# Kernel optimization log

Hardware: AMD Instinct MI355X
Metric: run time of the kernel (lower is better)

Reference implementation:

```python
import jax, jax.numpy as jnp
import numpy as np
from jax import lax

B, N, D, H, E, K, FF = 4, 1024, 1024, 16, 12, 2, 4
HD = D // H
EPS_LN = 1e-5


def setup_inputs() -> dict:
    key = jax.random.key(0)
    ks = jax.random.split(key, 10)
    s = 0.02
    return {
        "x": jax.random.normal(ks[0], (B, N, D), jnp.float32),
        "Wr": jax.random.normal(ks[1], (E, D), jnp.float32) * s,          # router [E, D] (no bias)
        "Wq": jax.random.normal(ks[2], (E, D, D), jnp.float32) * s,       # per-expert [out, in]
        "Wk": jax.random.normal(ks[3], (E, D, D), jnp.float32) * s,
        "Wv": jax.random.normal(ks[4], (E, D, D), jnp.float32) * s,
        "Wo": jax.random.normal(ks[5], (E, D, D), jnp.float32) * s,
        "W1": jax.random.normal(ks[6], (FF * D, D), jnp.float32) * s,
        "b1": jnp.zeros((FF * D,), jnp.float32),
        "W2": jax.random.normal(ks[7], (D, FF * D), jnp.float32) * s,
        "b2": jnp.zeros((D,), jnp.float32),
        "g1": jnp.ones((D,), jnp.float32),
        "be1": jnp.zeros((D,), jnp.float32),
        "g2": jnp.ones((D,), jnp.float32),
        "be2": jnp.zeros((D,), jnp.float32),
    }


def _ln(x, g, b):
    m = jnp.mean(x, axis=-1, keepdims=True)
    v = jnp.mean(jnp.square(x - m), axis=-1, keepdims=True)
    return (x - m) * lax.rsqrt(v + EPS_LN) * g + b


def _moe_mix(inp, W, combine):
    """sum_e combine[:, e] * (inp @ W[e].T) via scan over the E experts.
    inp: [T, Din], W: [E, Dout, Din], combine: [T, E] -> [T, Dout]"""
    def body(acc, ec):
        We, ce = ec
        return acc + ce[:, None] * (inp @ We.T), None
    acc0 = jnp.zeros((inp.shape[0], W.shape[1]), inp.dtype)
    acc, _ = lax.scan(body, acc0, (W, jnp.swapaxes(combine, 0, 1)))
    return acc


def _moe_attention(x, Wr, Wq, Wk, Wv, Wo):
    x_flat = x.reshape(-1, D)                     # [T, D]
    T = x_flat.shape[0]
    logits = x_flat @ Wr.T                        # [T, E]
    probs = jax.nn.softmax(logits, axis=-1)
    topv, topi = lax.top_k(probs, K)              # [T, K]
    topv = topv / (jnp.sum(topv, axis=-1, keepdims=True) + 1e-6)
    # dense combine weights [T, E] (zero for unselected experts)
    combine = jnp.zeros((T, E), x.dtype).at[jnp.arange(T)[:, None], topi].add(topv)

    q = _moe_mix(x_flat, Wq, combine)
    k = _moe_mix(x_flat, Wk, combine)
    v = _moe_mix(x_flat, Wv, combine)

    # [B, H, N, HD]
    q = q.reshape(B, N, H, HD).transpose(0, 2, 1, 3)
    k = k.reshape(B, N, H, HD).transpose(0, 2, 1, 3)
    v = v.reshape(B, N, H, HD).transpose(0, 2, 1, 3)
    scores = jnp.einsum("bhqd,bhkd->bhqk", q, k) / jnp.sqrt(jnp.asarray(HD, x.dtype))
    attn = jax.nn.softmax(scores, axis=-1)
    out = jnp.einsum("bhqk,bhkd->bhqd", attn, v)
    out_flat = out.transpose(0, 2, 1, 3).reshape(T, D)

    o = _moe_mix(out_flat, Wo, combine)           # expert output projection

    # load-balance loss (no grad in original: computed under torch.no_grad)
    counts = jnp.zeros((E,), x.dtype).at[topi.ravel()].add(1.0)
    p = probs.sum(axis=0)
    lb = jax.lax.stop_gradient((counts / (counts.sum() + 1e-6) * p).sum() * E)
    return o.reshape(B, N, D), lb


def reference(x, Wr, Wq, Wk, Wv, Wo, W1, b1, W2, b2, g1, be1, g2, be2):
    # pre-norm transformer block: x + MoEAttn(LN(x)); + FFN(LN(.))
    attn_out, lb = _moe_attention(_ln(x, g1, be1), Wr, Wq, Wk, Wv, Wo)
    h = x + attn_out
    hn = _ln(h, g2, be2)
    ff = (jax.nn.gelu(hn @ W1.T + b1)) @ W2.T + b2   # dropout=0 (eval)
    y = h + ff
    return y, lb
```

## Files before the change

kernel.cpp:

```cpp
#include <hip/hip_runtime.h>

#define B_ 4
#define N_ 1024
#define D_ 1024
#define H_ 16
#define HD_ 64
#define E_ 12
#define T_ 4096
#define FF_ 4096

static constexpr size_t SZ_ = (size_t)T_ * D_;

typedef __attribute__((ext_vector_type(8))) short bhalf8;
typedef __attribute__((ext_vector_type(4))) float f32x4;

#define GLDS(gp, lp)                                                         \
  __builtin_amdgcn_global_load_lds(                                          \
      (const __attribute__((address_space(1))) void*)(gp),                   \
      (__attribute__((address_space(3))) void*)(lp), 16, 0, 0)

__device__ __forceinline__ float wave_sum64(float v) {
#pragma unroll
  for (int o = 32; o > 0; o >>= 1) v += __shfl_down(v, o);
  return v;
}

__device__ __forceinline__ unsigned short f2bf(float f) {
  unsigned u = __float_as_uint(f);
  u += 0x7FFFu + ((u >> 16) & 1u);
  return (unsigned short)(u >> 16);
}
__device__ __forceinline__ float b2f(unsigned short s) {
  return __uint_as_float(((unsigned)s) << 16);
}
__device__ __forceinline__ unsigned addpair_bf(unsigned x, unsigned y) {
  float lo = b2f((unsigned short)(x & 0xffff)) + b2f((unsigned short)(y & 0xffff));
  float hi = b2f((unsigned short)(x >> 16)) + b2f((unsigned short)(y >> 16));
  return (unsigned)f2bf(lo) | ((unsigned)f2bf(hi) << 16);
}

__device__ __forceinline__ float gelu_f(float x) {
  float u = 0.7978845608028654f * (x + 0.044715f * x * x * x);
  u = fminf(fmaxf(u, -15.f), 15.f);
  float e = __expf(2.f * u);
  float th = (e - 1.f) / (e + 1.f);
  return 0.5f * x * (1.f + th);
}

__device__ __forceinline__ int slot_of(int row, int q) {
  return row * 4 + (q ^ ((row >> 1) & 3));
}

__global__ __launch_bounds__(256) void ln_kernel(const float* __restrict__ x,
    const float* __restrict__ g, const float* __restrict__ b,
    unsigned short* __restrict__ outb) {
  const int t = blockIdx.x, tid = threadIdx.x;
  const size_t base = (size_t)t * D_;
  const float4 v = ((const float4*)(x + base))[tid];
  float s = v.x + v.y + v.z + v.w;
  float s2 = v.x * v.x + v.y * v.y + v.z * v.z + v.w * v.w;
  s = wave_sum64(s);
  s2 = wave_sum64(s2);
  __shared__ float ls[4], ls2[4];
  const int w = tid >> 6;
  if ((tid & 63) == 0) { ls[w] = s; ls2[w] = s2; }
  __syncthreads();
  const float mean = (ls[0] + ls[1] + ls[2] + ls[3]) * (1.0f / D_);
  const float var = (ls2[0] + ls2[1] + ls2[2] + ls2[3]) * (1.0f / D_) - mean * mean;
  const float inv = rsqrtf(var + 1e-5f);
  const float4 gg = ((const float4*)g)[tid];
  const float4 bb = ((const float4*)b)[tid];
  ushort4 u4;
  u4.x = f2bf((v.x - mean) * inv * gg.x + bb.x);
  u4.y = f2bf((v.y - mean) * inv * gg.y + bb.y);
  u4.z = f2bf((v.z - mean) * inv * gg.z + bb.z);
  u4.w = f2bf((v.w - mean) * inv * gg.w + bb.w);
  ((ushort4*)(outb + base))[tid] = u4;
}

__global__ __launch_bounds__(256) void hln2_kernel(const float* __restrict__ x,
    const unsigned short* __restrict__ oa, const unsigned short* __restrict__ ob,
    const float* __restrict__ g, const float* __restrict__ be,
    const float* __restrict__ b2, float* __restrict__ y,
    unsigned short* __restrict__ hnb) {
  const int t = blockIdx.x, tid = threadIdx.x;
  const size_t base = (size_t)t * D_;
  const float4 xv = ((const float4*)(x + base))[tid];
  const ushort4 av = ((const ushort4*)(oa + base))[tid];
  const ushort4 bv = ((const ushort4*)(ob + base))[tid];
  float4 hv;
  hv.x = xv.x + b2f(av.x) + b2f(bv.x);
  hv.y = xv.y + b2f(av.y) + b2f(bv.y);
  hv.z = xv.z + b2f(av.z) + b2f(bv.z);
  hv.w = xv.w + b2f(av.w) + b2f(bv.w);
  const float4 b2v = ((const float4*)b2)[tid];
  float4 yv;
  yv.x = hv.x + b2v.x; yv.y = hv.y + b2v.y;
  yv.z = hv.z + b2v.z; yv.w = hv.w + b2v.w;
  ((float4*)(y + base))[tid] = yv;
  float s = hv.x + hv.y + hv.z + hv.w;
  float s2 = hv.x * hv.x + hv.y * hv.y + hv.z * hv.z + hv.w * hv.w;
  s = wave_sum64(s);
  s2 = wave_sum64(s2);
  __shared__ float ls[4], ls2[4];
  const int w = tid >> 6;
  if ((tid & 63) == 0) { ls[w] = s; ls2[w] = s2; }
  __syncthreads();
  const float mean = (ls[0] + ls[1] + ls[2] + ls[3]) * (1.0f / D_);
  const float var = (ls2[0] + ls2[1] + ls2[2] + ls2[3]) * (1.0f / D_) - mean * mean;
  const float inv = rsqrtf(var + 1e-5f);
  const float4 gg = ((const float4*)g)[tid];
  const float4 bb = ((const float4*)be)[tid];
  ushort4 o4;
  o4.x = f2bf((hv.x - mean) * inv * gg.x + bb.x);
  o4.y = f2bf((hv.y - mean) * inv * gg.y + bb.y);
  o4.z = f2bf((hv.z - mean) * inv * gg.z + bb.z);
  o4.w = f2bf((hv.w - mean) * inv * gg.w + bb.w);
  ((ushort4*)(hnb + base))[tid] = o4;
}

__global__ __launch_bounds__(256) void router_ln(const float* __restrict__ x,
    const float* __restrict__ g, const float* __restrict__ b,
    const float* __restrict__ Wr, float* __restrict__ probs,
    int* __restrict__ topi, float2* __restrict__ topw) {
  const int t = blockIdx.x, tid = threadIdx.x;
  const float4 xv = ((const float4*)(x + (size_t)t * D_))[tid];
  float s = xv.x + xv.y + xv.z + xv.w;
  float s2 = xv.x * xv.x + xv.y * xv.y + xv.z * xv.z + xv.w * xv.w;
  s = wave_sum64(s);
  s2 = wave_sum64(s2);
  __shared__ float ls[4], ls2[4];
  const int w = tid >> 6;
  if ((tid & 63) == 0) { ls[w] = s; ls2[w] = s2; }
  __syncthreads();
  const float mean = (ls[0] + ls[1] + ls[2] + ls[3]) * (1.0f / D_);
  const float var = (ls2[0] + ls2[1] + ls2[2] + ls2[3]) * (1.0f / D_) - mean * mean;
  const float inv = rsqrtf(var + 1e-5f);
  const float4 gg = ((const float4*)g)[tid];
  const float4 bb = ((const float4*)b)[tid];
  float4 xn4;
  xn4.x = (xv.x - mean) * inv * gg.x + bb.x;
  xn4.y = (xv.y - mean) * inv * gg.y + bb.y;
  xn4.z = (xv.z - mean) * inv * gg.z + bb.z;
  xn4.w = (xv.w - mean) * inv * gg.w + bb.w;
  float acc[E_];
#pragma unroll
  for (int e = 0; e < E_; ++e) {
    const float4 wv = ((const float4*)(Wr + (size_t)e * D_))[tid];
    acc[e] = xn4.x * wv.x + xn4.y * wv.y + xn4.z * wv.z + xn4.w * wv.w;
  }
#pragma unroll
  for (int e = 0; e < E_; ++e) acc[e] = wave_sum64(acc[e]);
  __shared__ float red[4][E_];
  if ((tid & 63) == 0) {
#pragma unroll
    for (int e = 0; e < E_; ++e) red[w][e] = acc[e];
  }
  __syncthreads();
  if (tid == 0) {
    float lg[E_];
    float mx = -1e30f;
#pragma unroll
    for (int e = 0; e < E_; ++e) {
      lg[e] = red[0][e] + red[1][e] + red[2][e] + red[3][e];
      mx = fmaxf(mx, lg[e]);
    }
    float p[E_];
    float sum = 0.f;
#pragma unroll
    for (int e = 0; e < E_; ++e) { p[e] = __expf(lg[e] - mx); sum += p[e]; }
    const float invs = 1.f / sum;
#pragma unroll
    for (int e = 0; e < E_; ++e) {
      p[e] *= invs;
      probs[t * E_ + e] = p[e];
    }
    int i0 = 0;
#pragma unroll
    for (int e = 1; e < E_; ++e) if (p[e] > p[i0]) i0 = e;
    int i1 = (i0 == 0) ? 1 : 0;
#pragma unroll
    for (int e = 0; e < E_; ++e) if (e != i0 && p[e] > p[i1]) i1 = e;
    const float rs = 1.f / (p[i0] + p[i1] + 1e-6f);
    topi[t] = i0 | (i1 << 8);
    topw[t] = make_float2(p[i0] * rs, p[i1] * rs);
  }
}

__global__ __launch_bounds__(256) void psum_kernel(const float* __restrict__ probs,
                                                   float* __restrict__ psum) {
  const int tid = threadIdx.x;
  float local[E_] = {};
  for (int t = tid; t < T_; t += 256) {
#pragma unroll
    for (int e = 0; e < E_; ++e) local[e] += probs[t * E_ + e];
  }
#pragma unroll
  for (int e = 0; e < E_; ++e) local[e] = wave_sum64(local[e]);
  __shared__ float red[4][E_];
  const int w = tid >> 6;
  if ((tid & 63) == 0) {
#pragma unroll
    for (int e = 0; e < E_; ++e) red[w][e] = local[e];
  }
  __syncthreads();
  if (tid < E_)
    psum[tid] = red[0][tid] + red[1][tid] + red[2][tid] + red[3][tid];
}

__global__ __launch_bounds__(256) void build_lists(const int* __restrict__ topi,
    const float2* __restrict__ topw, int* __restrict__ ecnt,
    int* __restrict__ etok, float* __restrict__ ewt) {
  const int e = blockIdx.x;
  const int tid = threadIdx.x;
  const int wid = tid >> 6, lane = tid & 63;
  __shared__ int wbase[4];
  __shared__ int base;
  if (tid == 0) base = 0;
  __syncthreads();
  for (int c = 0; c < T_; c += 256) {
    const int t = c + tid;
    const int pk = topi[t];
    const int i0 = pk & 0xFF, i1 = (pk >> 8) & 0xFF;
    const float2 w2 = topw[t];
    const int sel = (i0 == e) ? 0 : ((i1 == e) ? 1 : -1);
    const unsigned long long mask = __ballot(sel >= 0);
    const int prefix = __popcll(mask & ((1ULL << lane) - 1ULL));
    if (lane == 0) wbase[wid] = __popcll(mask);
    __syncthreads();
    if (tid == 0) {
      int s = base;
#pragma unroll
      for (int ww = 0; ww < 4; ++ww) { int cc = wbase[ww]; wbase[ww] = s; s += cc; }
      base = s;
    }
    __syncthreads();
    if (sel >= 0) {
      const int pos = wbase[wid] + prefix;
      etok[e * T_ + pos] = t | (sel << 16);
      ewt[e * T_ + pos] = sel ? w2.y : w2.x;
    }
    __syncthreads();
  }
  if (tid == 0) ecnt[e] = base;
}

__global__ __launch_bounds__(256) void cvtw_kernel(const float* __restrict__ src,
    unsigned short* __restrict__ dst) {
  const size_t i = (size_t)blockIdx.x * 256 + threadIdx.x;
  const float4 v = ((const float4*)src)[i];
  ushort4 o;
  o.x = f2bf(v.x); o.y = f2bf(v.y); o.z = f2bf(v.z); o.w = f2bf(v.w);
  ((ushort4*)dst)[i] = o;
}

__global__ __launch_bounds__(256) void moe_mfma(const unsigned short* __restrict__ Ab,
    const unsigned short* __restrict__ Wb, unsigned short* __restrict__ out,
    size_t kkStride, const int* __restrict__ ecnt, const int* __restrict__ etok,
    const float* __restrict__ ewt) {
  const int e = blockIdx.z;
  const int Me = ecnt[e];
  const int m0 = blockIdx.y * 128;
  if (m0 >= Me) return;
  const int n0 = blockIdx.x * 128;
  const unsigned short* W = Wb + (size_t)e * D_ * D_;
  __shared__ __align__(16) unsigned short As[128 * 32];
  __shared__ __align__(16) unsigned short Bs[128 * 32];
  __shared__ int stok[128];
  __shared__ float swt[128];
  const int tid = threadIdx.x;
  if (tid < 128) {
    const int s = m0 + tid;
    if (s < Me) { stok[tid] = etok[e * T_ + s]; swt[tid] = ewt[e * T_ + s]; }
    else        { stok[tid] = 0;                swt[tid] = 0.f; }
  }
  __syncthreads();
  const int s0 = tid, s1 = tid + 256;
  const int r0 = s0 >> 2, q0 = (s0 & 3) ^ ((r0 >> 1) & 3);
  const int r1 = s1 >> 2, q1 = (s1 & 3) ^ ((r1 >> 1) & 3);
  const unsigned short* aP0 = Ab + (size_t)(stok[r0] & 0xFFFF) * D_ + q0 * 8;
  const unsigned short* aP1 = Ab + (size_t)(stok[r1] & 0xFFFF) * D_ + q1 * 8;
  const unsigned short* bP0 = W + (size_t)(n0 + r0) * D_ + q0 * 8;
  const unsigned short* bP1 = W + (size_t)(n0 + r1) * D_ + q1 * 8;
  char* AsC = (char*)As;
  char* BsC = (char*)Bs;
  const int wave = tid >> 6, lane = tid & 63;
  const int wm0 = (wave >> 1) * 64, wn0 = (wave & 1) * 64;
  const int lr = lane & 15, lq = lane >> 4;
  int aoff[4], boff[4];
#pragma unroll
  for (int t = 0; t < 4; ++t) {
    aoff[t] = slot_of(wm0 + t * 16 + lr, lq) * 16;
    boff[t] = slot_of(wn0 + t * 16 + lr, lq) * 16;
  }
  f32x4 acc[4][4];
#pragma unroll
  for (int i = 0; i < 4; ++i)
#pragma unroll
    for (int j = 0; j < 4; ++j) acc[i][j] = (f32x4){0.f, 0.f, 0.f, 0.f};
  for (int kt = 0; kt < D_; kt += 32) {
    __syncthreads();
    GLDS(aP0 + kt, AsC + s0 * 16);
    GLDS(aP1 + kt, AsC + s1 * 16);
    GLDS(bP0 + kt, BsC + s0 * 16);
    GLDS(bP1 + kt, BsC + s1 * 16);
    __syncthreads();
    bhalf8 af[4], bfr[4];
#pragma unroll
    for (int t = 0; t < 4; ++t) af[t] = *(const bhalf8*)(AsC + aoff[t]);
#pragma unroll
    for (int t = 0; t < 4; ++t) bfr[t] = *(const bhalf8*)(BsC + boff[t]);
#pragma unroll
    for (int i = 0; i < 4; ++i)
#pragma unroll
      for (int j = 0; j < 4; ++j)
        acc[i][j] = __builtin_amdgcn_mfma_f32_16x16x32_bf16(af[i], bfr[j], acc[i][j], 0, 0, 0);
  }
#pragma unroll
  for (int mt = 0; mt < 4; ++mt)
#pragma unroll
    for (int nt = 0; nt < 4; ++nt) {
      const f32x4 c = acc[mt][nt];
      const int col = n0 + wn0 + nt * 16 + lr;
#pragma unroll
      for (int r = 0; r < 4; ++r) {
        const int row = wm0 + mt * 16 + lq * 4 + r;
        if (m0 + row < Me) {
          const int pk = stok[row];
          out[(size_t)(pk >> 16) * kkStride + (size_t)(pk & 0xFFFF) * D_ + col] =
              f2bf(c[r] * swt[row]);
        }
      }
    }
}

__global__ __launch_bounds__(256) void ffn1_mfma(const unsigned short* __restrict__ Ab,
    const unsigned short* __restrict__ Bb, const float* __restrict__ bias,
    unsigned short* __restrict__ mid) {
  const int m0 = blockIdx.y * 128, n0 = blockIdx.x * 128;
  __shared__ __align__(16) unsigned short As[128 * 32];
  __shared__ __align__(16) unsigned short Bs[128 * 32];
  const int tid = threadIdx.x;
  const int s0 = tid, s1 = tid + 256;
  const int r0 = s0 >> 2, q0 = (s0 & 3) ^ ((r0 >> 1) & 3);
  const int r1 = s1 >> 2, q1 = (s1 & 3) ^ ((r1 >> 1) & 3);
  const unsigned short* aP0 = Ab + (size_t)(m0 + r0) * D_ + q0 * 8;
  const unsigned short* aP1 = Ab + (size_t)(m0 + r1) * D_ + q1 * 8;
  const unsigned short* bP0 = Bb + (size_t)(n0 + r0) * D_ + q0 * 8;
  const unsigned short* bP1 = Bb + (size_t)(n0 + r1) * D_ + q1 * 8;
  char* AsC = (char*)As;
  char* BsC = (char*)Bs;
  const int wave = tid >> 6, lane = tid & 63;
  const int wm0 = (wave >> 1) * 64, wn0 = (wave & 1) * 64;
  const int lr = lane & 15, lq = lane >> 4;
  int aoff[4], boff[4];
#pragma unroll
  for (int t = 0; t < 4; ++t) {
    aoff[t] = slot_of(wm0 + t * 16 + lr, lq) * 16;
    boff[t] = slot_of(wn0 + t * 16 + lr, lq) * 16;
  }
  f32x4 acc[4][4];
#pragma unroll
  for (int i = 0; i < 4; ++i)
#pragma unroll
    for (int j = 0; j < 4; ++j) acc[i][j] = (f32x4){0.f, 0.f, 0.f, 0.f};
  for (int kt = 0; kt < D_; kt += 32) {
    __syncthreads();
    GLDS(aP0 + kt, AsC + s0 * 16);
    GLDS(aP1 + kt, AsC + s1 * 16);
    GLDS(bP0 + kt, BsC + s0 * 16);
    GLDS(bP1 + kt, BsC + s1 * 16);
    __syncthreads();
    bhalf8 af[4], bfr[4];
#pragma unroll
    for (int t = 0; t < 4; ++t) af[t] = *(const bhalf8*)(AsC + aoff[t]);
#pragma unroll
    for (int t = 0; t < 4; ++t) bfr[t] = *(const bhalf8*)(BsC + boff[t]);
#pragma unroll
    for (int i = 0; i < 4; ++i)
#pragma unroll
      for (int j = 0; j < 4; ++j)
        acc[i][j] = __builtin_amdgcn_mfma_f32_16x16x32_bf16(af[i], bfr[j], acc[i][j], 0, 0, 0);
  }
  float bcol[4];
#pragma unroll
  for (int nt = 0; nt < 4; ++nt) bcol[nt] = bias[n0 + wn0 + nt * 16 + lr];
#pragma unroll
  for (int mt = 0; mt < 4; ++mt)
#pragma unroll
    for (int nt = 0; nt < 4; ++nt) {
      const f32x4 c = acc[mt][nt];
      const int col = n0 + wn0 + nt * 16 + lr;
#pragma unroll
      for (int r = 0; r < 4; ++r) {
        const int row = m0 + wm0 + mt * 16 + lq * 4 + r;
        mid[(size_t)row * FF_ + col] = f2bf(gelu_f(c[r] + bcol[nt]));
      }
    }
}

__global__ __launch_bounds__(256) void ffn2_split(const unsigned short* __restrict__ Ab,
    const unsigned short* __restrict__ Bb, float* __restrict__ part0,
    float* __restrict__ part1) {
  const int m0 = blockIdx.y * 128, n0 = blockIdx.x * 128;
  const int k0 = blockIdx.z * (FF_ / 2);
  float* const part = blockIdx.z ? part1 : part0;
  __shared__ __align__(16) unsigned short As[128 * 32];
  __shared__ __align__(16) unsigned short Bs[128 * 32];
  const int tid = threadIdx.x;
  const int s0 = tid, s1 = tid + 256;
  const int r0 = s0 >> 2, q0 = (s0 & 3) ^ ((r0 >> 1) & 3);
  const int r1 = s1 >> 2, q1 = (s1 & 3) ^ ((r1 >> 1) & 3);
  const unsigned short* aP0 = Ab + (size_t)(m0 + r0) * FF_ + q0 * 8 + k0;
  const unsigned short* aP1 = Ab + (size_t)(m0 + r1) * FF_ + q1 * 8 + k0;
  const unsigned short* bP0 = Bb + (size_t)(n0 + r0) * FF_ + q0 * 8 + k0;
  const unsigned short* bP1 = Bb + (size_t)(n0 + r1) * FF_ + q1 * 8 + k0;
  char* AsC = (char*)As;
  char* BsC = (char*)Bs;
  const int wave = tid >> 6, lane = tid & 63;
  const int wm0 = (wave >> 1) * 64, wn0 = (wave & 1) * 64;
  const int lr = lane & 15, lq = lane >> 4;
  int aoff[4], boff[4];
#pragma unroll
  for (int t = 0; t < 4; ++t) {
    aoff[t] = slot_of(wm0 + t * 16 + lr, lq) * 16;
    boff[t] = slot_of(wn0 + t * 16 + lr, lq) * 16;
  }
  f32x4 acc[4][4];
#pragma unroll
  for (int i = 0; i < 4; ++i)
#pragma unroll
    for (int j = 0; j < 4; ++j) acc[i][j] = (f32x4){0.f, 0.f, 0.f, 0.f};
  for (int kt = 0; kt < FF_ / 2; kt += 32) {
    __syncthreads();
    GLDS(aP0 + kt, AsC + s0 * 16);
    GLDS(aP1 + kt, AsC + s1 * 16);
    GLDS(bP0 + kt, BsC + s0 * 16);
    GLDS(bP1 + kt, BsC + s1 * 16);
    __syncthreads();
    bhalf8 af[4], bfr[4];
#pragma unroll
    for (int t = 0; t < 4; ++t) af[t] = *(const bhalf8*)(AsC + aoff[t]);
#pragma unroll
    for (int t = 0; t < 4; ++t) bfr[t] = *(const bhalf8*)(BsC + boff[t]);
#pragma unroll
    for (int i = 0; i < 4; ++i)
#pragma unroll
      for (int j = 0; j < 4; ++j)
        acc[i][j] = __builtin_amdgcn_mfma_f32_16x16x32_bf16(af[i], bfr[j], acc[i][j], 0, 0, 0);
  }
#pragma unroll
  for (int mt = 0; mt < 4; ++mt)
#pragma unroll
    for (int nt = 0; nt < 4; ++nt) {
      const f32x4 c = acc[mt][nt];
      const int col = n0 + wn0 + nt * 16 + lr;
#pragma unroll
      for (int r = 0; r < 4; ++r) {
        const int row = m0 + wm0 + mt * 16 + lq * 4 + r;
        part[(size_t)row * D_ + col] = c[r];
      }
    }
}

__global__ __launch_bounds__(256) void add3_kernel(float* __restrict__ y,
    const float* __restrict__ p0, const float* __restrict__ p1) {
  const size_t i = (size_t)blockIdx.x * 256 + threadIdx.x;
  const float4 a = ((const float4*)y)[i];
  const float4 u = ((const float4*)p0)[i];
  const float4 v = ((const float4*)p1)[i];
  float4 o;
  o.x = a.x + u.x + v.x;
  o.y = a.y + u.y + v.y;
  o.z = a.z + u.z + v.z;
  o.w = a.w + u.w + v.w;
  ((float4*)y)[i] = o;
}

__global__ __launch_bounds__(256) void add2b_kernel(unsigned short* __restrict__ a,
    const unsigned short* __restrict__ b) {
  const size_t i = (size_t)blockIdx.x * 256 + threadIdx.x;
  uint4 av = ((uint4*)a)[i];
  const uint4 bv = ((const uint4*)b)[i];
  av.x = addpair_bf(av.x, bv.x);
  av.y = addpair_bf(av.y, bv.y);
  av.z = addpair_bf(av.z, bv.z);
  av.w = addpair_bf(av.w, bv.w);
  ((uint4*)a)[i] = av;
}

__global__ __launch_bounds__(256) void attn_kernel(const unsigned short* __restrict__ q,
    const unsigned short* __restrict__ k, const unsigned short* __restrict__ v,
    unsigned short* __restrict__ out) {
  const int bh = blockIdx.x;
  const int b = bh >> 4, h = bh & 15;
  const int q0 = blockIdx.y * 64;
  const int tid = threadIdx.x;
  const int wave = tid >> 6, lane = tid & 63;
  const int lc = lane & 15, lg = lane >> 4;

  __shared__ __align__(16) unsigned short Ks[64 * 64];
  __shared__ __align__(16) unsigned short Vt[64 * 64];
  __shared__ __align__(16) unsigned short Pl[4][16 * 64];
  char* const KsC = (char*)Ks;
  char* const VtC = (char*)Vt;
  char* const PlC = (char*)&Pl[wave][0];

  bhalf8 qf0, qf1;
  {
    const unsigned short* qp =
        q + ((size_t)(b * N_ + q0 + wave * 16 + lc)) * D_ + h * HD_ + lg * 8;
    qf0 = *(const bhalf8*)qp;
    qf1 = *(const bhalf8*)(qp + 32);
  }

  int off[4][2];
#pragma unroll
  for (int t = 0; t < 4; ++t)
#pragma unroll
    for (int ch = 0; ch < 2; ++ch)
      off[t][ch] = (t * 16 + lc) * 128 + (((ch * 4 + lg) ^ (lc & 7)) << 4);

  const int krow = tid >> 2, ks0 = tid & 3;
  const unsigned short* const kgp =
      k + ((size_t)(b * N_ + krow)) * D_ + h * HD_ + ks0 * 8;
  const int kwo0 = krow * 128 + ((ks0 ^ (krow & 7)) << 4);
  const int kwo1 = krow * 128 + (((ks0 ^ 4) ^ (krow & 7)) << 4);
  const int vkv = (tid & 31) * 2, vd0 = (tid >> 5) * 8;
  const unsigned short* const vgp =
      v + ((size_t)(b * N_ + vkv)) * D_ + h * HD_ + vd0;
  int vwo[8];
#pragma unroll
  for (int c = 0; c < 8; ++c) {
    const int d = vd0 + c;
    vwo[c] = d * 128 + ((((vkv >> 3) ^ (d & 7)) << 4)) + (vkv & 7) * 2;
  }

  float m_i[4], l_i[4];
  f32x4 o_acc[4];
#pragma unroll
  for (int r = 0; r < 4; ++r) { m_i[r] = -3.0e38f; l_i[r] = 0.f; }
#pragma unroll
  for (int t = 0; t < 4; ++t) o_acc[t] = (f32x4){0.f, 0.f, 0.f, 0.f};

  uint4 ka = *(const uint4*)(kgp);
  uint4 kb = *(const uint4*)(kgp + 32);
  uint4 va = *(const uint4*)(vgp);
  uint4 vb = *(const uint4*)(vgp + D_);

  for (int kt = 0; kt < 16; ++kt) {
    __syncthreads();
    *(uint4*)(KsC + kwo0) = ka;
    *(uint4*)(KsC + kwo1) = kb;
    {
      const unsigned av4[4] = {va.x, va.y, va.z, va.w};
      const unsigned bv4[4] = {vb.x, vb.y, vb.z, vb.w};
#pragma unroll
      for (int c = 0; c < 4; ++c) {
        const unsigned w0 = (av4[c] & 0xffffu) | (bv4[c] << 16);
        const unsigned w1 = (av4[c] >> 16) | (bv4[c] & 0xffff0000u);
        *(unsigned*)(VtC + vwo[2 * c]) = w0;
        *(unsigned*)(VtC + vwo[2 * c + 1]) = w1;
      }
    }
    __syncthreads();
    if (kt < 15) {
      const size_t go = (size_t)(kt + 1) * 64 * D_;
      ka = *(const uint4*)(kgp + go);
      kb = *(const uint4*)(kgp + go + 32);
      va = *(const uint4*)(vgp + go);
      vb = *(const uint4*)(vgp + go + D_);
    }
    f32x4 s4[4];
#pragma unroll
    for (int t = 0; t < 4; ++t) {
      f32x4 acc = (f32x4){0.f, 0.f, 0.f, 0.f};
      acc = __builtin_amdgcn_mfma_f32_16x16x32_bf16(
          qf0, *(const bhalf8*)(KsC + off[t][0]), acc, 0, 0, 0);
      acc = __builtin_amdgcn_mfma_f32_16x16x32_bf16(
          qf1, *(const bhalf8*)(KsC + off[t][1]), acc, 0, 0, 0);
      s4[t] = acc;
    }
    float alpha[4];
#pragma unroll
    for (int r = 0; r < 4; ++r) {
      const float e0 = s4[0][r] * 0.125f, e1 = s4[1][r] * 0.125f;
      const float e2 = s4[2][r] * 0.125f, e3 = s4[3][r] * 0.125f;
      float mt = fmaxf(fmaxf(e0, e1), fmaxf(e2, e3));
#pragma unroll
      for (int o = 8; o > 0; o >>= 1) mt = fmaxf(mt, __shfl_xor(mt, o));
      const float mn = fmaxf(m_i[r], mt);
      alpha[r] = __expf(m_i[r] - mn);
      m_i[r] = mn;
      const float p0 = __expf(e0 - mn), p1 = __expf(e1 - mn);
      const float p2 = __expf(e2 - mn), p3 = __expf(e3 - mn);
      float rs = p0 + p1 + p2 + p3;
#pragma unroll
      for (int o = 8; o > 0; o >>= 1) rs += __shfl_xor(rs, o);
      l_i[r] = l_i[r] * alpha[r] + rs;
      const int qrow = 4 * lg + r;
      const int rb = qrow * 128 + (lc & 7) * 2;
      const int sw = qrow & 7;
      *(unsigned short*)(PlC + rb + (((0 + (lc >> 3)) ^ sw) << 4)) = f2bf(p0);
      *(unsigned short*)(PlC + rb + (((2 + (lc >> 3)) ^ sw) << 4)) = f2bf(p1);
      *(unsigned short*)(PlC + rb + (((4 + (lc >> 3)) ^ sw) << 4)) = f2bf(p2);
      *(unsigned short*)(PlC + rb + (((6 + (lc >> 3)) ^ sw) << 4)) = f2bf(p3);
    }
#pragma unroll
    for (int t = 0; t < 4; ++t) {
      f32x4 o = o_acc[t];
      o[0] *= alpha[0]; o[1] *= alpha[1]; o[2] *= alpha[2]; o[3] *= alpha[3];
      o_acc[t] = o;
    }
    const bhalf8 pf0 = *(const bhalf8*)(PlC + off[0][0]);
    const bhalf8 pf1 = *(const bhalf8*)(PlC + off[0][1]);
#pragma unroll
    for (int t = 0; t < 4; ++t) {
      o_acc[t] = __builtin_amdgcn_mfma_f32_16x16x32_bf16(
          pf0, *(const bhalf8*)(VtC + off[t][0]), o_acc[t], 0, 0, 0);
      o_acc[t] = __builtin_amdgcn_mfma_f32_16x16x32_bf16(
          pf1, *(const bhalf8*)(VtC + off[t][1]), o_acc[t], 0, 0, 0);
    }
  }
  const size_t obase = ((size_t)(b * N_ + q0 + wave * 16)) * D_ + h * HD_;
#pragma unroll
  for (int r = 0; r < 4; ++r) {
    const float inv = 1.f / l_i[r];
    const size_t rbase = obase + (size_t)(4 * lg + r) * D_;
#pragma unroll
    for (int t = 0; t < 4; ++t)
      out[rbase + t * 16 + lc] = f2bf(o_acc[t][r] * inv);
  }
}

__global__ void lb_kernel(const int* __restrict__ ecnt,
                          const float* __restrict__ psum, float* __restrict__ out) {
  if (threadIdx.x == 0 && blockIdx.x == 0) {
    float tot = 0.f;
    for (int e = 0; e < E_; ++e) tot += (float)ecnt[e];
    float s = 0.f;
    for (int e = 0; e < E_; ++e) s += (float)ecnt[e] / (tot + 1e-6f) * psum[e];
    out[0] = s * (float)E_;
  }
}

extern "C" void kernel_launch(void* const* d_in, const int* in_sizes, int n_in,
                              void* d_out, int out_size, void* d_ws, size_t ws_size,
                              hipStream_t stream) {
  (void)in_sizes; (void)n_in; (void)out_size; (void)ws_size;
  const float* x  = (const float*)d_in[0];
  const float* Wr = (const float*)d_in[1];
  const float* Wq = (const float*)d_in[2];
  const float* Wk = (const float*)d_in[3];
  const float* Wv = (const float*)d_in[4];
  const float* Wo = (const float*)d_in[5];
  const float* W1 = (const float*)d_in[6];
  const float* b1 = (const float*)d_in[7];
  const float* W2 = (const float*)d_in[8];
  const float* b2 = (const float*)d_in[9];
  const float* g1 = (const float*)d_in[10];
  const float* be1 = (const float*)d_in[11];
  const float* g2 = (const float*)d_in[12];
  const float* be2 = (const float*)d_in[13];
  float* y = (float*)d_out;

  char* p = (char*)d_ws;
  unsigned short* Rb = (unsigned short*)p;   p += (size_t)E_ * D_ * D_ * 2;
  unsigned short* xnb = (unsigned short*)p;  p += SZ_ * 2;
  unsigned short* q2b = (unsigned short*)p;  p += 2 * SZ_ * 2;
  unsigned short* k2b = (unsigned short*)p;  p += 2 * SZ_ * 2;
  unsigned short* v2b = (unsigned short*)p;  p += 2 * SZ_ * 2;
  unsigned short* W1b = (unsigned short*)p;  p += (size_t)FF_ * D_ * 2;
  unsigned short* W2b = (unsigned short*)p;  p += (size_t)FF_ * D_ * 2;
  float* psum = (float*)p;               p += E_ * 4;
  int* ecnt = (int*)p;                   p += E_ * 4;
  int* etok = (int*)p;                   p += (size_t)E_ * T_ * 4;
  float* ewt = (float*)p;                p += (size_t)E_ * T_ * 4;
  float* probs = (float*)p;              p += (size_t)T_ * E_ * 4;
  int* topi = (int*)p;                   p += T_ * 4;
  float2* topw = (float2*)p;
  unsigned short* attb = v2b + SZ_;
  unsigned short* o2b  = q2b;
  unsigned short* hnb  = v2b;
  float* part0         = (float*)k2b;
  float* part1         = (float*)v2b;
  unsigned short* midb = (unsigned short*)d_ws;

  ln_kernel<<<T_, 256, 0, stream>>>(x, g1, be1, xnb);
  cvtw_kernel<<<(FF_ * D_) / 1024, 256, 0, stream>>>(W1, W1b);
  cvtw_kernel<<<(FF_ * D_) / 1024, 256, 0, stream>>>(W2, W2b);
  router_ln<<<T_, 256, 0, stream>>>(x, g1, be1, Wr, probs, topi, topw);
  psum_kernel<<<1, 256, 0, stream>>>(probs, psum);
  build_lists<<<E_, 256, 0, stream>>>(topi, topw, ecnt, etok, ewt);
  dim3 gmoe(D_ / 128, T_ / 128, E_);
  const int gw = (E_ * D_ * D_) / 1024;
  cvtw_kernel<<<gw, 256, 0, stream>>>(Wq, Rb);
  moe_mfma<<<gmoe, 256, 0, stream>>>(xnb, Rb, q2b, SZ_, ecnt, etok, ewt);
  cvtw_kernel<<<gw, 256, 0, stream>>>(Wk, Rb);
  moe_mfma<<<gmoe, 256, 0, stream>>>(xnb, Rb, k2b, SZ_, ecnt, etok, ewt);
  cvtw_kernel<<<gw, 256, 0, stream>>>(Wv, Rb);
  moe_mfma<<<gmoe, 256, 0, stream>>>(xnb, Rb, v2b, SZ_, ecnt, etok, ewt);
  cvtw_kernel<<<gw, 256, 0, stream>>>(Wo, Rb);
  add2b_kernel<<<SZ_ / 2048, 256, 0, stream>>>(q2b, q2b + SZ_);
  add2b_kernel<<<SZ_ / 2048, 256, 0, stream>>>(k2b, k2b + SZ_);
  add2b_kernel<<<SZ_ / 2048, 256, 0, stream>>>(v2b, v2b + SZ_);
  attn_kernel<<<dim3(B_ * H_, N_ / 64), 256, 0, stream>>>(q2b, k2b, v2b, attb);
  moe_mfma<<<gmoe, 256, 0, stream>>>(attb, Rb, o2b, SZ_, ecnt, etok, ewt);
  hln2_kernel<<<T_, 256, 0, stream>>>(x, o2b, o2b + SZ_, g2, be2, b2, y, hnb);
  ffn1_mfma<<<dim3(FF_ / 128, T_ / 128), 256, 0, stream>>>(hnb, W1b, b1, midb);
  ffn2_split<<<dim3(D_ / 128, T_ / 128, 2), 256, 0, stream>>>(midb, W2b, part0, part1);
  add3_kernel<<<SZ_ / 1024, 256, 0, stream>>>(y, part0, part1);
  lb_kernel<<<1, 64, 0, stream>>>(ecnt, psum, y + SZ_);
}
```

Before: 680.8 us.

## Shrink MoE GEMM M-tile, split FFN2 K four ways, merge bf16 adds

```diff
diff --git a/kernel.cpp b/kernel.cpp
--- a/kernel.cpp
+++ b/kernel.cpp
@@ -260,71 +260,69 @@
     const float* __restrict__ ewt) {
   const int e = blockIdx.z;
   const int Me = ecnt[e];
-  const int m0 = blockIdx.y * 128;
+  const int m0 = blockIdx.y * 64;
   if (m0 >= Me) return;
   const int n0 = blockIdx.x * 128;
   const unsigned short* W = Wb + (size_t)e * D_ * D_;
-  __shared__ __align__(16) unsigned short As[128 * 32];
+  __shared__ __align__(16) unsigned short As[64 * 32];
   __shared__ __align__(16) unsigned short Bs[128 * 32];
-  __shared__ int stok[128];
-  __shared__ float swt[128];
+  __shared__ int stok[64];
+  __shared__ float swt[64];
   const int tid = threadIdx.x;
-  if (tid < 128) {
+  if (tid < 64) {
     const int s = m0 + tid;
     if (s < Me) { stok[tid] = etok[e * T_ + s]; swt[tid] = ewt[e * T_ + s]; }
     else        { stok[tid] = 0;                swt[tid] = 0.f; }
   }
   __syncthreads();
+  const int ra = tid >> 2, qa = (tid & 3) ^ ((ra >> 1) & 3);
   const int s0 = tid, s1 = tid + 256;
-  const int r0 = s0 >> 2, q0 = (s0 & 3) ^ ((r0 >> 1) & 3);
-  const int r1 = s1 >> 2, q1 = (s1 & 3) ^ ((r1 >> 1) & 3);
-  const unsigned short* aP0 = Ab + (size_t)(stok[r0] & 0xFFFF) * D_ + q0 * 8;
-  const unsigned short* aP1 = Ab + (size_t)(stok[r1] & 0xFFFF) * D_ + q1 * 8;
-  const unsigned short* bP0 = W + (size_t)(n0 + r0) * D_ + q0 * 8;
-  const unsigned short* bP1 = W + (size_t)(n0 + r1) * D_ + q1 * 8;
+  const int rb0 = s0 >> 2, qb0 = (s0 & 3) ^ ((rb0 >> 1) & 3);
+  const int rb1 = s1 >> 2, qb1 = (s1 & 3) ^ ((rb1 >> 1) & 3);
+  const unsigned short* aP  = Ab + (size_t)(stok[ra] & 0xFFFF) * D_ + qa * 8;
+  const unsigned short* bP0 = W + (size_t)(n0 + rb0) * D_ + qb0 * 8;
+  const unsigned short* bP1 = W + (size_t)(n0 + rb1) * D_ + qb1 * 8;
   char* AsC = (char*)As;
   char* BsC = (char*)Bs;
   const int wave = tid >> 6, lane = tid & 63;
-  const int wm0 = (wave >> 1) * 64, wn0 = (wave & 1) * 64;
+  const int wn0 = wave * 32;
   const int lr = lane & 15, lq = lane >> 4;
-  int aoff[4], boff[4];
-#pragma unroll
-  for (int t = 0; t < 4; ++t) {
-    aoff[t] = slot_of(wm0 + t * 16 + lr, lq) * 16;
-    boff[t] = slot_of(wn0 + t * 16 + lr, lq) * 16;
-  }
-  f32x4 acc[4][4];
+  int aoff[4], boff[2];
+#pragma unroll
+  for (int t = 0; t < 4; ++t) aoff[t] = slot_of(t * 16 + lr, lq) * 16;
+#pragma unroll
+  for (int t = 0; t < 2; ++t) boff[t] = slot_of(wn0 + t * 16 + lr, lq) * 16;
+  f32x4 acc[4][2];
 #pragma unroll
   for (int i = 0; i < 4; ++i)
 #pragma unroll
-    for (int j = 0; j < 4; ++j) acc[i][j] = (f32x4){0.f, 0.f, 0.f, 0.f};
+    for (int j = 0; j < 2; ++j) acc[i][j] = (f32x4){0.f, 0.f, 0.f, 0.f};
   for (int kt = 0; kt < D_; kt += 32) {
     __syncthreads();
-    GLDS(aP0 + kt, AsC + s0 * 16);
-    GLDS(aP1 + kt, AsC + s1 * 16);
+    GLDS(aP + kt, AsC + tid * 16);
     GLDS(bP0 + kt, BsC + s0 * 16);
     GLDS(bP1 + kt, BsC + s1 * 16);
     __syncthreads();
-    bhalf8 af[4], bfr[4];
+    bhalf8 af[4], bfr[2];
 #pragma unroll
     for (int t = 0; t < 4; ++t) af[t] = *(const bhalf8*)(AsC + aoff[t]);
 #pragma unroll
-    for (int t = 0; t < 4; ++t) bfr[t] = *(const bhalf8*)(BsC + boff[t]);
+    for (int t = 0; t < 2; ++t) bfr[t] = *(const bhalf8*)(BsC + boff[t]);
 #pragma unroll
     for (int i = 0; i < 4; ++i)
 #pragma unroll
-      for (int j = 0; j < 4; ++j)
+      for (int j = 0; j < 2; ++j)
         acc[i][j] = __builtin_amdgcn_mfma_f32_16x16x32_bf16(af[i], bfr[j], acc[i][j], 0, 0, 0);
   }
 #pragma unroll
   for (int mt = 0; mt < 4; ++mt)
 #pragma unroll
-    for (int nt = 0; nt < 4; ++nt) {
+    for (int nt = 0; nt < 2; ++nt) {
       const f32x4 c = acc[mt][nt];
       const int col = n0 + wn0 + nt * 16 + lr;
 #pragma unroll
       for (int r = 0; r < 4; ++r) {
-        const int row = wm0 + mt * 16 + lq * 4 + r;
+        const int row = mt * 16 + lq * 4 + r;
         if (m0 + row < Me) {
           const int pk = stok[row];
           out[(size_t)(pk >> 16) * kkStride + (size_t)(pk & 0xFFFF) * D_ + col] =
@@ -399,12 +397,14 @@
     }
 }
 
-__global__ __launch_bounds__(256) void ffn2_split(const unsigned short* __restrict__ Ab,
-    const unsigned short* __restrict__ Bb, float* __restrict__ part0,
-    float* __restrict__ part1) {
+__global__ __launch_bounds__(256) void ffn2_split4(const unsigned short* __restrict__ Ab,
+    const unsigned short* __restrict__ Bb, float* __restrict__ y,
+    float* __restrict__ p1, float* __restrict__ p2, float* __restrict__ p3) {
   const int m0 = blockIdx.y * 128, n0 = blockIdx.x * 128;
-  const int k0 = blockIdx.z * (FF_ / 2);
-  float* const part = blockIdx.z ? part1 : part0;
+  const int z = blockIdx.z;
+  const int k0 = z * (FF_ / 4);
+  float* const dst = (z == 0) ? y : ((z == 1) ? p1 : ((z == 2) ? p2 : p3));
+  const bool rmw = (z == 0);
   __shared__ __align__(16) unsigned short As[128 * 32];
   __shared__ __align__(16) unsigned short Bs[128 * 32];
   const int tid = threadIdx.x;
@@ -431,7 +431,7 @@
   for (int i = 0; i < 4; ++i)
 #pragma unroll
     for (int j = 0; j < 4; ++j) acc[i][j] = (f32x4){0.f, 0.f, 0.f, 0.f};
-  for (int kt = 0; kt < FF_ / 2; kt += 32) {
+  for (int kt = 0; kt < FF_ / 4; kt += 32) {
     __syncthreads();
     GLDS(aP0 + kt, AsC + s0 * 16);
     GLDS(aP1 + kt, AsC + s1 * 16);
@@ -458,28 +458,35 @@
 #pragma unroll
       for (int r = 0; r < 4; ++r) {
         const int row = m0 + wm0 + mt * 16 + lq * 4 + r;
-        part[(size_t)row * D_ + col] = c[r];
+        const size_t idx = (size_t)row * D_ + col;
+        if (rmw) dst[idx] += c[r];
+        else     dst[idx] = c[r];
       }
     }
 }
 
-__global__ __launch_bounds__(256) void add3_kernel(float* __restrict__ y,
-    const float* __restrict__ p0, const float* __restrict__ p1) {
+__global__ __launch_bounds__(256) void addf_kernel(float* __restrict__ y,
+    const float* __restrict__ p1, const float* __restrict__ p2,
+    const float* __restrict__ p3) {
   const size_t i = (size_t)blockIdx.x * 256 + threadIdx.x;
   const float4 a = ((const float4*)y)[i];
-  const float4 u = ((const float4*)p0)[i];
-  const float4 v = ((const float4*)p1)[i];
+  const float4 u = ((const float4*)p1)[i];
+  const float4 v = ((const float4*)p2)[i];
+  const float4 w = ((const float4*)p3)[i];
   float4 o;
-  o.x = a.x + u.x + v.x;
-  o.y = a.y + u.y + v.y;
-  o.z = a.z + u.z + v.z;
-  o.w = a.w + u.w + v.w;
+  o.x = a.x + u.x + v.x + w.x;
+  o.y = a.y + u.y + v.y + w.y;
+  o.z = a.z + u.z + v.z + w.z;
+  o.w = a.w + u.w + v.w + w.w;
   ((float4*)y)[i] = o;
 }
 
-__global__ __launch_bounds__(256) void add2b_kernel(unsigned short* __restrict__ a,
-    const unsigned short* __restrict__ b) {
-  const size_t i = (size_t)blockIdx.x * 256 + threadIdx.x;
+__global__ __launch_bounds__(256) void add2b3_kernel(unsigned short* __restrict__ base) {
+  const int reg = blockIdx.x >> 11;
+  const int ib = blockIdx.x & 2047;
+  unsigned short* a = base + (size_t)reg * 2 * SZ_;
+  const unsigned short* b = a + SZ_;
+  const size_t i = (size_t)ib * 256 + threadIdx.x;
   uint4 av = ((uint4*)a)[i];
   const uint4 bv = ((const uint4*)b)[i];
   av.x = addpair_bf(av.x, bv.x);
@@ -682,8 +689,9 @@
   unsigned short* attb = v2b + SZ_;
   unsigned short* o2b  = q2b;
   unsigned short* hnb  = v2b;
-  float* part0         = (float*)k2b;
-  float* part1         = (float*)v2b;
+  float* part1         = (float*)k2b;
+  float* part2         = (float*)v2b;
+  float* part3         = (float*)q2b;
   unsigned short* midb = (unsigned short*)d_ws;
 
   ln_kernel<<<T_, 256, 0, stream>>>(x, g1, be1, xnb);
@@ -692,7 +700,7 @@
   router_ln<<<T_, 256, 0, stream>>>(x, g1, be1, Wr, probs, topi, topw);
   psum_kernel<<<1, 256, 0, stream>>>(probs, psum);
   build_lists<<<E_, 256, 0, stream>>>(topi, topw, ecnt, etok, ewt);
-  dim3 gmoe(D_ / 128, T_ / 128, E_);
+  dim3 gmoe(D_ / 128, T_ / 64, E_);
   const int gw = (E_ * D_ * D_) / 1024;
   cvtw_kernel<<<gw, 256, 0, stream>>>(Wq, Rb);
   moe_mfma<<<gmoe, 256, 0, stream>>>(xnb, Rb, q2b, SZ_, ecnt, etok, ewt);
@@ -701,14 +709,12 @@
   cvtw_kernel<<<gw, 256, 0, stream>>>(Wv, Rb);
   moe_mfma<<<gmoe, 256, 0, stream>>>(xnb, Rb, v2b, SZ_, ecnt, etok, ewt);
   cvtw_kernel<<<gw, 256, 0, stream>>>(Wo, Rb);
-  add2b_kernel<<<SZ_ / 2048, 256, 0, stream>>>(q2b, q2b + SZ_);
-  add2b_kernel<<<SZ_ / 2048, 256, 0, stream>>>(k2b, k2b + SZ_);
-  add2b_kernel<<<SZ_ / 2048, 256, 0, stream>>>(v2b, v2b + SZ_);
+  add2b3_kernel<<<3 * (SZ_ / 2048), 256, 0, stream>>>(q2b);
   attn_kernel<<<dim3(B_ * H_, N_ / 64), 256, 0, stream>>>(q2b, k2b, v2b, attb);
   moe_mfma<<<gmoe, 256, 0, stream>>>(attb, Rb, o2b, SZ_, ecnt, etok, ewt);
   hln2_kernel<<<T_, 256, 0, stream>>>(x, o2b, o2b + SZ_, g2, be2, b2, y, hnb);
   ffn1_mfma<<<dim3(FF_ / 128, T_ / 128), 256, 0, stream>>>(hnb, W1b, b1, midb);
-  ffn2_split<<<dim3(D_ / 128, T_ / 128, 2), 256, 0, stream>>>(midb, W2b, part0, part1);
-  add3_kernel<<<SZ_ / 1024, 256, 0, stream>>>(y, part0, part1);
+  ffn2_split4<<<dim3(D_ / 128, T_ / 128, 4), 256, 0, stream>>>(midb, W2b, y, part1, part2, part3);
+  addf_kernel<<<SZ_ / 1024, 256, 0, stream>>>(y, part1, part2, part3);
   lb_kernel<<<1, 64, 0, stream>>>(ecnt, psum, y + SZ_);
 }
```

Result: slower. 718.7 us (+5.6%).

## Batch Q/K/V weight conversion and MoE projections into single launches

Applied to the files above, without the earlier changes.

```diff
diff --git a/kernel.cpp b/kernel.cpp
--- a/kernel.cpp
+++ b/kernel.cpp
@@ -254,16 +254,32 @@
   ((ushort4*)dst)[i] = o;
 }
 
+__global__ __launch_bounds__(256) void cvtw3_kernel(const float* __restrict__ a,
+    const float* __restrict__ b, const float* __restrict__ c,
+    unsigned short* __restrict__ dst) {
+  const int gw = (E_ * D_ * D_) / 1024;
+  const int r = blockIdx.x / gw;
+  const int ib = blockIdx.x - r * gw;
+  const float* src = (r == 0) ? a : ((r == 1) ? b : c);
+  const size_t i = (size_t)ib * 256 + threadIdx.x;
+  const float4 v = ((const float4*)src)[i];
+  ushort4 o;
+  o.x = f2bf(v.x); o.y = f2bf(v.y); o.z = f2bf(v.z); o.w = f2bf(v.w);
+  ((ushort4*)(dst + (size_t)r * E_ * D_ * D_))[i] = o;
+}
+
 __global__ __launch_bounds__(256) void moe_mfma(const unsigned short* __restrict__ Ab,
-    const unsigned short* __restrict__ Wb, unsigned short* __restrict__ out,
-    size_t kkStride, const int* __restrict__ ecnt, const int* __restrict__ etok,
+    const unsigned short* __restrict__ Wb, unsigned short* __restrict__ outb,
+    const int* __restrict__ ecnt, const int* __restrict__ etok,
     const float* __restrict__ ewt) {
   const int e = blockIdx.z;
   const int Me = ecnt[e];
   const int m0 = blockIdx.y * 128;
   if (m0 >= Me) return;
-  const int n0 = blockIdx.x * 128;
-  const unsigned short* W = Wb + (size_t)e * D_ * D_;
+  const int proj = blockIdx.x >> 3;
+  const int n0 = (blockIdx.x & 7) * 128;
+  const unsigned short* W = Wb + ((size_t)proj * E_ + e) * D_ * D_;
+  unsigned short* out = outb + (size_t)proj * 2 * SZ_;
   __shared__ __align__(16) unsigned short As[128 * 32];
   __shared__ __align__(16) unsigned short Bs[128 * 32];
   __shared__ int stok[128];
@@ -327,7 +343,7 @@
         const int row = wm0 + mt * 16 + lq * 4 + r;
         if (m0 + row < Me) {
           const int pk = stok[row];
-          out[(size_t)(pk >> 16) * kkStride + (size_t)(pk & 0xFFFF) * D_ + col] =
+          out[(size_t)(pk >> 16) * SZ_ + (size_t)(pk & 0xFFFF) * D_ + col] =
               f2bf(c[r] * swt[row]);
         }
       }
@@ -477,9 +493,12 @@
   ((float4*)y)[i] = o;
 }
 
-__global__ __launch_bounds__(256) void add2b_kernel(unsigned short* __restrict__ a,
-    const unsigned short* __restrict__ b) {
-  const size_t i = (size_t)blockIdx.x * 256 + threadIdx.x;
+__global__ __launch_bounds__(256) void add2b3_kernel(unsigned short* __restrict__ base) {
+  const int reg = blockIdx.x >> 11;
+  const int ib = blockIdx.x & 2047;
+  unsigned short* a = base + (size_t)reg * 2 * SZ_;
+  const unsigned short* b = a + SZ_;
+  const size_t i = (size_t)ib * 256 + threadIdx.x;
   uint4 av = ((uint4*)a)[i];
   const uint4 bv = ((const uint4*)b)[i];
   av.x = addpair_bf(av.x, bv.x);
@@ -647,7 +666,7 @@
 extern "C" void kernel_launch(void* const* d_in, const int* in_sizes, int n_in,
                               void* d_out, int out_size, void* d_ws, size_t ws_size,
                               hipStream_t stream) {
-  (void)in_sizes; (void)n_in; (void)out_size; (void)ws_size;
+  (void)in_sizes; (void)n_in; (void)out_size;
   const float* x  = (const float*)d_in[0];
   const float* Wr = (const float*)d_in[1];
   const float* Wq = (const float*)d_in[2];
@@ -664,48 +683,69 @@
   const float* be2 = (const float*)d_in[13];
   float* y = (float*)d_out;
 
+  const bool big = ws_size >= (size_t)136 * 1024 * 1024;
   char* p = (char*)d_ws;
-  unsigned short* Rb = (unsigned short*)p;   p += (size_t)E_ * D_ * D_ * 2;
-  unsigned short* xnb = (unsigned short*)p;  p += SZ_ * 2;
-  unsigned short* q2b = (unsigned short*)p;  p += 2 * SZ_ * 2;
-  unsigned short* k2b = (unsigned short*)p;  p += 2 * SZ_ * 2;
-  unsigned short* v2b = (unsigned short*)p;  p += 2 * SZ_ * 2;
-  unsigned short* W1b = (unsigned short*)p;  p += (size_t)FF_ * D_ * 2;
-  unsigned short* W2b = (unsigned short*)p;  p += (size_t)FF_ * D_ * 2;
-  float* psum = (float*)p;               p += E_ * 4;
-  int* ecnt = (int*)p;                   p += E_ * 4;
-  int* etok = (int*)p;                   p += (size_t)E_ * T_ * 4;
-  float* ewt = (float*)p;                p += (size_t)E_ * T_ * 4;
-  float* probs = (float*)p;              p += (size_t)T_ * E_ * 4;
-  int* topi = (int*)p;                   p += T_ * 4;
-  float2* topw = (float2*)p;
+  unsigned short *Rb, *xnb, *q2b, *WoB, *W1b, *W2b, *midb;
+  char* tail;
+  if (big) {
+    Rb  = (unsigned short*)p;
+    xnb = (unsigned short*)(p + 75497472);
+    q2b = (unsigned short*)(p + 75497472 + 8388608);
+    tail = p + 75497472 + 8388608 + 6 * SZ_ * 2;
+    WoB  = Rb;
+    W1b  = (unsigned short*)(p + 25165824);
+    W2b  = (unsigned short*)(p + 33554432);
+    midb = (unsigned short*)(p + 41943040);
+  } else {
+    Rb  = (unsigned short*)p;
+    xnb = (unsigned short*)(p + 25165824);
+    q2b = xnb + SZ_;
+    W1b = q2b + 6 * SZ_;
+    W2b = W1b + (size_t)FF_ * D_;
+    tail = (char*)(W2b + (size_t)FF_ * D_);
+    WoB  = Rb;
+    midb = (unsigned short*)d_ws;
+  }
+  unsigned short* k2b = q2b + 2 * SZ_;
+  unsigned short* v2b = k2b + 2 * SZ_;
+  float* psum = (float*)tail;            tail += E_ * 4;
+  int* ecnt = (int*)tail;                tail += E_ * 4;
+  int* etok = (int*)tail;                tail += (size_t)E_ * T_ * 4;
+  float* ewt = (float*)tail;             tail += (size_t)E_ * T_ * 4;
+  float* probs = (float*)tail;           tail += (size_t)T_ * E_ * 4;
+  int* topi = (int*)tail;                tail += T_ * 4;
+  float2* topw = (float2*)tail;
   unsigned short* attb = v2b + SZ_;
   unsigned short* o2b  = q2b;
   unsigned short* hnb  = v2b;
   float* part0         = (float*)k2b;
   float* part1         = (float*)v2b;
-  unsigned short* midb = (unsigned short*)d_ws;
-
+
+  const int gw = (E_ * D_ * D_) / 1024;
   ln_kernel<<<T_, 256, 0, stream>>>(x, g1, be1, xnb);
-  cvtw_kernel<<<(FF_ * D_) / 1024, 256, 0, stream>>>(W1, W1b);
-  cvtw_kernel<<<(FF_ * D_) / 1024, 256, 0, stream>>>(W2, W2b);
   router_ln<<<T_, 256, 0, stream>>>(x, g1, be1, Wr, probs, topi, topw);
   psum_kernel<<<1, 256, 0, stream>>>(probs, psum);
   build_lists<<<E_, 256, 0, stream>>>(topi, topw, ecnt, etok, ewt);
-  dim3 gmoe(D_ / 128, T_ / 128, E_);
-  const int gw = (E_ * D_ * D_) / 1024;
-  cvtw_kernel<<<gw, 256, 0, stream>>>(Wq, Rb);
-  moe_mfma<<<gmoe, 256, 0, stream>>>(xnb, Rb, q2b, SZ_, ecnt, etok, ewt);
-  cvtw_kernel<<<gw, 256, 0, stream>>>(Wk, Rb);
-  moe_mfma<<<gmoe, 256, 0, stream>>>(xnb, Rb, k2b, SZ_, ecnt, etok, ewt);
-  cvtw_kernel<<<gw, 256, 0, stream>>>(Wv, Rb);
-  moe_mfma<<<gmoe, 256, 0, stream>>>(xnb, Rb, v2b, SZ_, ecnt, etok, ewt);
-  cvtw_kernel<<<gw, 256, 0, stream>>>(Wo, Rb);
-  add2b_kernel<<<SZ_ / 2048, 256, 0, stream>>>(q2b, q2b + SZ_);
-  add2b_kernel<<<SZ_ / 2048, 256, 0, stream>>>(k2b, k2b + SZ_);
-  add2b_kernel<<<SZ_ / 2048, 256, 0, stream>>>(v2b, v2b + SZ_);
+  if (big) {
+    cvtw3_kernel<<<3 * gw, 256, 0, stream>>>(Wq, Wk, Wv, Rb);
+    moe_mfma<<<dim3(24, T_ / 128, E_), 256, 0, stream>>>(xnb, Rb, q2b, ecnt, etok, ewt);
+    cvtw_kernel<<<gw, 256, 0, stream>>>(Wo, WoB);
+    cvtw_kernel<<<(FF_ * D_) / 1024, 256, 0, stream>>>(W1, W1b);
+    cvtw_kernel<<<(FF_ * D_) / 1024, 256, 0, stream>>>(W2, W2b);
+  } else {
+    cvtw_kernel<<<(FF_ * D_) / 1024, 256, 0, stream>>>(W1, W1b);
+    cvtw_kernel<<<(FF_ * D_) / 1024, 256, 0, stream>>>(W2, W2b);
+    cvtw_kernel<<<gw, 256, 0, stream>>>(Wq, Rb);
+    moe_mfma<<<dim3(8, T_ / 128, E_), 256, 0, stream>>>(xnb, Rb, q2b, ecnt, etok, ewt);
+    cvtw_kernel<<<gw, 256, 0, stream>>>(Wk, Rb);
+    moe_mfma<<<dim3(8, T_ / 128, E_), 256, 0, stream>>>(xnb, Rb, k2b, ecnt, etok, ewt);
+    cvtw_kernel<<<gw, 256, 0, stream>>>(Wv, Rb);
+    moe_mfma<<<dim3(8, T_ / 128, E_), 256, 0, stream>>>(xnb, Rb, v2b, ecnt, etok, ewt);
+    cvtw_kernel<<<gw, 256, 0, stream>>>(Wo, Rb);
+  }
+  add2b3_kernel<<<3 * (SZ_ / 2048), 256, 0, stream>>>(q2b);
   attn_kernel<<<dim3(B_ * H_, N_ / 64), 256, 0, stream>>>(q2b, k2b, v2b, attb);
-  moe_mfma<<<gmoe, 256, 0, stream>>>(attb, Rb, o2b, SZ_, ecnt, etok, ewt);
+  moe_mfma<<<dim3(8, T_ / 128, E_), 256, 0, stream>>>(attb, WoB, o2b, ecnt, etok, ewt);
   hln2_kernel<<<T_, 256, 0, stream>>>(x, o2b, o2b + SZ_, g2, be2, b2, y, hnb);
   ffn1_mfma<<<dim3(FF_ / 128, T_ / 128), 256, 0, stream>>>(hnb, W1b, b1, midb);
   ffn2_split<<<dim3(D_ / 128, T_ / 128, 2), 256, 0, stream>>>(midb, W2b, part0, part1);
```

After: 627.7 us. 1.08x faster.
